# Optimization experiments

Hardware: AMD Instinct MI355X
Metric: run time of the kernel (lower is better)

Reference implementation:

```python
import jax, jax.numpy as jnp
import numpy as np

TOK = 256        # flattened batch*seq tokens (decode-style, memory-bound)
IN_F = 4096
OUT_F = 4096
N_OUTLIER = 32


def quantize_rowwise(x):
    """Symmetric rowwise int8 quantization: scale = rowwise absmax."""
    scale = jnp.max(jnp.abs(x), axis=-1)                      # [rows]
    safe = jnp.maximum(scale, 1e-8)
    q = jnp.clip(jnp.round(x / safe[:, None] * 127.0), -127.0, 127.0)
    return q, scale


def setup_inputs() -> dict:
    key = jax.random.key(0)
    k1, k2, k3, k4, k5 = jax.random.split(key, 5)
    x = jax.random.normal(k1, (TOK, IN_F), jnp.float32)
    weight_int8 = jax.random.randint(k2, (OUT_F, IN_F), -127, 128, jnp.int32)
    weight_scales = jax.random.uniform(k3, (OUT_F,), jnp.float32, minval=0.5, maxval=2.0)
    # spread unique outlier column indices across in_features
    outlier_indices = jnp.arange(N_OUTLIER, dtype=jnp.int32) * (IN_F // N_OUTLIER)
    outlier_weights = jax.random.normal(k4, (OUT_F, N_OUTLIER), jnp.float32) * 0.02
    bias = jax.random.normal(k5, (OUT_F,), jnp.float32) * 0.01
    # from_linear zeros outlier columns of the int8 weight before quantization
    weight_int8 = weight_int8.at[:, outlier_indices].set(0)
    return {"x": x, "weight_int8": weight_int8, "weight_scales": weight_scales,
            "outlier_indices": outlier_indices, "outlier_weights": outlier_weights,
            "bias": bias}


def reference(x, weight_int8, weight_scales, outlier_indices, outlier_weights, bias):
    # _forward_mixed: outlier columns handled in fp, rest quantize->dequant int8.
    # Selecting the non-outlier columns is equivalent to zeroing the outlier
    # columns (the dropped weight columns contribute 0 to the GEMM, and the
    # rowwise absmax scale is unaffected since |0| = 0). This keeps shapes
    # static and jit-friendly while computing identical math.
    in_f = x.shape[-1]
    mask = jnp.ones((in_f,), dtype=bool).at[outlier_indices].set(False)

    x_main = x * mask                                         # [T, in]
    xq, xs = quantize_rowwise(x_main)                         # int8-valued fp, [T]
    x_fp = xq * (xs[:, None] / 127.0)                         # dequantized activations

    w_fp = (weight_int8 * mask).astype(jnp.float32) * (weight_scales[:, None] / 127.0)  # [out, in]
    out_main = x_fp @ w_fp.T                                  # [T, out]

    x_outlier = x[:, outlier_indices]                         # [T, n_out]
    out_outlier = x_outlier @ outlier_weights.T               # [T, out]

    return out_main + out_outlier + bias
```

## Files before the change

### kernel.cpp

```cpp
#include <hip/hip_runtime.h>
#include <stdint.h>

#define TOK 256
#define IN_F 4096
#define OUT_F 4096
#define N_OUT 32

#define BN 16
#define MACRO_K 512
#define NMACRO (IN_F / MACRO_K)
#define KSTEPS (MACRO_K / 64)

typedef int v4i __attribute__((ext_vector_type(4)));

__global__ __launch_bounds__(256) void oal_quant(
    const float* __restrict__ x, const int* __restrict__ oidx,
    int8_t* __restrict__ xq, float* __restrict__ xs, float* __restrict__ xo)
{
    const int row = blockIdx.x;
    const int tid = threadIdx.x;
    __shared__ unsigned char flags[IN_F];
    __shared__ float wmax[4];
    __shared__ float s_scale;

    *reinterpret_cast<uint4*>(&flags[tid * 16]) = make_uint4(0u, 0u, 0u, 0u);
    __syncthreads();
    if (tid < N_OUT) flags[oidx[tid]] = 1;
    __syncthreads();

    const float* xr = x + (size_t)row * IN_F;
    float4 v[4];
    const float4* xp = reinterpret_cast<const float4*>(xr + tid * 16);
    #pragma unroll
    for (int i = 0; i < 4; ++i) v[i] = xp[i];

    uint4 f = *reinterpret_cast<const uint4*>(&flags[tid * 16]);
    unsigned int fw[4] = { f.x, f.y, f.z, f.w };
    float vals[16];
    #pragma unroll
    for (int i = 0; i < 4; ++i) {
        vals[i*4+0] = ((fw[i]      ) & 255u) ? 0.0f : v[i].x;
        vals[i*4+1] = ((fw[i] >>  8) & 255u) ? 0.0f : v[i].y;
        vals[i*4+2] = ((fw[i] >> 16) & 255u) ? 0.0f : v[i].z;
        vals[i*4+3] = ((fw[i] >> 24) & 255u) ? 0.0f : v[i].w;
    }

    float m = 0.0f;
    #pragma unroll
    for (int i = 0; i < 16; ++i) m = fmaxf(m, fabsf(vals[i]));
    #pragma unroll
    for (int off = 32; off > 0; off >>= 1) m = fmaxf(m, __shfl_xor(m, off, 64));
    const int lane = tid & 63, wid = tid >> 6;
    if (lane == 0) wmax[wid] = m;
    __syncthreads();
    if (tid == 0) {
        float s = fmaxf(fmaxf(wmax[0], wmax[1]), fmaxf(wmax[2], wmax[3]));
        s_scale = s;
        xs[row] = s;
    }
    __syncthreads();
    const float safe = fmaxf(s_scale, 1e-8f);

    int q[16];
    #pragma unroll
    for (int i = 0; i < 16; ++i) {
        float t = vals[i] / safe * 127.0f;
        t = fminf(127.0f, fmaxf(-127.0f, rintf(t)));
        q[i] = (int)t;
    }
    uint4 packed;
    unsigned int* pw = &packed.x;
    #pragma unroll
    for (int i = 0; i < 4; ++i)
        pw[i] = (unsigned)(q[i*4] & 255) | ((unsigned)(q[i*4+1] & 255) << 8)
              | ((unsigned)(q[i*4+2] & 255) << 16) | ((unsigned)(q[i*4+3] & 255) << 24);
    *reinterpret_cast<uint4*>(xq + (size_t)row * IN_F + tid * 16) = packed;

    if (tid < N_OUT) xo[row * N_OUT + tid] = xr[oidx[tid]];
}

__global__ __launch_bounds__(512, 2) void oal_gemm(
    const int8_t* __restrict__ xq, const int* __restrict__ w,
    const float* __restrict__ xs, const float* __restrict__ wscale,
    const float* __restrict__ ow, const float* __restrict__ bias,
    const float* __restrict__ xo, float* __restrict__ out)
{
    const int bn = blockIdx.x;
    const int tid = threadIdx.x;
    const int lane = tid & 63;
    const int wv = tid >> 6;

    __shared__ __align__(16) signed char Bs[2][BN][528];
    __shared__ __align__(16) float XO[TOK][N_OUT];

    {
        const float4* src = reinterpret_cast<const float4*>(xo);
        float4* dst = reinterpret_cast<float4*>(&XO[0][0]);
        #pragma unroll
        for (int i = 0; i < 4; ++i) dst[tid * 4 + i] = src[tid * 4 + i];
    }

    const int sr = tid >> 5;
    const int sc = tid & 31;
    const int* wbase = w + (size_t)(bn * BN + sr) * IN_F + sc * 16;

    int4 wr_[4];
    auto load_regs = [&](int mm) {
        const int4* p = reinterpret_cast<const int4*>(wbase + mm * MACRO_K);
        #pragma unroll
        for (int i = 0; i < 4; ++i) wr_[i] = p[i];
    };
    auto pack_store = [&](int buf) {
        int p[4];
        #pragma unroll
        for (int i = 0; i < 4; ++i) {
            int4 a = wr_[i];
            p[i] = (a.x & 255) | ((a.y & 255) << 8) | ((a.z & 255) << 16) | ((a.w & 255) << 24);
        }
        *reinterpret_cast<int4*>(&Bs[buf][sr][sc * 16]) = make_int4(p[0], p[1], p[2], p[3]);
    };

    const int mrow = wv * 32;
    const int koff_lane = (lane >> 4) * 16;
    const int8_t* a0p = xq + (size_t)(mrow + (lane & 15)) * IN_F + koff_lane;
    const int8_t* a1p = a0p + 16 * IN_F;

    v4i acc0 = {0, 0, 0, 0}, acc1 = {0, 0, 0, 0};

    load_regs(0);
    pack_store(0);
    load_regs(1);
    __syncthreads();

    #pragma unroll
    for (int mm = 0; mm < NMACRO; ++mm) {
        const int cur = mm & 1;
        #pragma unroll
        for (int kk = 0; kk < KSTEPS; ++kk) {
            const int kg = mm * MACRO_K + kk * 64;
            v4i av0 = *reinterpret_cast<const v4i*>(a0p + kg);
            v4i av1 = *reinterpret_cast<const v4i*>(a1p + kg);
            v4i bv  = *reinterpret_cast<const v4i*>(&Bs[cur][lane & 15][kk * 64 + koff_lane]);
            acc0 = __builtin_amdgcn_mfma_i32_16x16x64_i8(av0, bv, acc0, 0, 0, 0);
            acc1 = __builtin_amdgcn_mfma_i32_16x16x64_i8(av1, bv, acc1, 0, 0, 0);
        }
        if (mm < NMACRO - 1) {
            pack_store(cur ^ 1);
            if (mm < NMACRO - 2) load_regs(mm + 2);
            __syncthreads();
        }
    }

    const int ocol = bn * BN + (lane & 15);
    const float wsc = wscale[ocol] * (1.0f / 16129.0f);
    const float bo  = bias[ocol];
    float4 owr[8];
    const float4* owp = reinterpret_cast<const float4*>(ow + (size_t)ocol * N_OUT);
    #pragma unroll
    for (int i = 0; i < 8; ++i) owr[i] = owp[i];

    const int rbase = (lane >> 4) * 4;
    #pragma unroll
    for (int mt = 0; mt < 2; ++mt) {
        v4i a = mt ? acc1 : acc0;
        #pragma unroll
        for (int r = 0; r < 4; ++r) {
            const int t = mrow + mt * 16 + rbase + r;
            const float* xr2 = &XO[t][0];
            float dot = 0.0f;
            #pragma unroll
            for (int j = 0; j < 8; ++j) {
                float4 o4 = owr[j];
                dot += xr2[j*4+0]*o4.x + xr2[j*4+1]*o4.y + xr2[j*4+2]*o4.z + xr2[j*4+3]*o4.w;
            }
            out[(size_t)t * OUT_F + ocol] = (float)a[r] * (xs[t] * wsc) + bo + dot;
        }
    }
}

extern "C" void kernel_launch(void* const* d_in, const int* in_sizes, int n_in,
                              void* d_out, int out_size, void* d_ws, size_t ws_size,
                              hipStream_t stream) {
    const float* x      = (const float*)d_in[0];
    const int*   w      = (const int*)  d_in[1];
    const float* wscale = (const float*)d_in[2];
    const int*   oidx   = (const int*)  d_in[3];
    const float* ow     = (const float*)d_in[4];
    const float* bias   = (const float*)d_in[5];
    float* out = (float*)d_out;

    int8_t* xq = (int8_t*)d_ws;
    float*  xs = (float*)((char*)d_ws + (size_t)TOK * IN_F);
    float*  xo = (float*)((char*)d_ws + (size_t)TOK * IN_F + 1024);

    oal_quant<<<TOK, 256, 0, stream>>>(x, oidx, xq, xs, xo);
    oal_gemm<<<OUT_F / BN, 512, 0, stream>>>(xq, w, xs, wscale, ow, bias, xo, out);
}
```

Baseline: 138.8 us.

## Split-K int8 GEMM with 128-wide tiles, LDS direct loads, separate epilogue

Replaces the 16-column-per-block GEMM with 128x256 tiles split eight ways along K (256 blocks). Activations are quantized into a pre-tiled layout and streamed into LDS with global_load_lds, and weights are packed into a swizzled LDS layout. The kernel uses 32x32x32 int8 MFMAs with a 2x2 fragment per wave. Partial int32 sums go to workspace, or are atomically added into the output if workspace is too small, and a new epilogue kernel applies the scales, outlier dot product and bias. This improves weight and activation reuse and parallelism, at the cost of extra partial-sum traffic (8x the output size) and one more kernel launch.

```diff
diff --git a/kernel.cpp b/kernel.cpp
--- a/kernel.cpp
+++ b/kernel.cpp
@@ -6,16 +6,17 @@
 #define OUT_F 4096
 #define N_OUT 32
 
-#define BN 16
-#define MACRO_K 512
-#define NMACRO (IN_F / MACRO_K)
-#define KSTEPS (MACRO_K / 64)
-
-typedef int v4i __attribute__((ext_vector_type(4)));
+typedef int v4i  __attribute__((ext_vector_type(4)));
+typedef int v16i __attribute__((ext_vector_type(16)));
+
+__device__ __forceinline__ void gll16(const void* g, void* l) {
+    __builtin_amdgcn_global_load_lds((const __attribute__((address_space(1))) void*)g,
+                                     (__attribute__((address_space(3))) void*)l, 16, 0, 0);
+}
 
 __global__ __launch_bounds__(256) void oal_quant(
     const float* __restrict__ x, const int* __restrict__ oidx,
-    int8_t* __restrict__ xq, float* __restrict__ xs, float* __restrict__ xo)
+    int8_t* __restrict__ xqt, float* __restrict__ xs, float* __restrict__ xo)
 {
     const int row = blockIdx.x;
     const int tid = threadIdx.x;
@@ -23,16 +24,16 @@
     __shared__ float wmax[4];
     __shared__ float s_scale;
 
-    *reinterpret_cast<uint4*>(&flags[tid * 16]) = make_uint4(0u, 0u, 0u, 0u);
-    __syncthreads();
-    if (tid < N_OUT) flags[oidx[tid]] = 1;
-    __syncthreads();
-
     const float* xr = x + (size_t)row * IN_F;
     float4 v[4];
     const float4* xp = reinterpret_cast<const float4*>(xr + tid * 16);
     #pragma unroll
     for (int i = 0; i < 4; ++i) v[i] = xp[i];
+
+    *reinterpret_cast<uint4*>(&flags[tid * 16]) = make_uint4(0u, 0u, 0u, 0u);
+    __syncthreads();
+    if (tid < N_OUT) flags[oidx[tid]] = 1;
+    __syncthreads();
 
     uint4 f = *reinterpret_cast<const uint4*>(&flags[tid * 16]);
     unsigned int fw[4] = { f.x, f.y, f.z, f.w };
@@ -74,107 +75,170 @@
     for (int i = 0; i < 4; ++i)
         pw[i] = (unsigned)(q[i*4] & 255) | ((unsigned)(q[i*4+1] & 255) << 8)
               | ((unsigned)(q[i*4+2] & 255) << 16) | ((unsigned)(q[i*4+3] & 255) << 24);
-    *reinterpret_cast<uint4*>(xq + (size_t)row * IN_F + tid * 16) = packed;
+
+    const int ks32  = tid >> 1;
+    const int khalf = tid & 1;
+    const int rowgrp = row >> 5;
+    *reinterpret_cast<uint4*>(xqt + (size_t)ks32 * 8192 + rowgrp * 1024
+                              + (khalf * 32 + (row & 31)) * 16) = packed;
 
     if (tid < N_OUT) xo[row * N_OUT + tid] = xr[oidx[tid]];
 }
 
-__global__ __launch_bounds__(512, 2) void oal_gemm(
-    const int8_t* __restrict__ xq, const int* __restrict__ w,
+template<int MODE>
+__global__ __launch_bounds__(512, 1) void oal_gemm(
+    const int8_t* __restrict__ xqt, const int* __restrict__ wgt,
+    int* __restrict__ pout)
+{
+    __shared__ __align__(16) int8_t sm[131072];
+    int8_t* As = sm;
+    int8_t* Bs = sm + 65536;
+
+    const int bn = blockIdx.x;
+    const int ntile = bn & 31, kslice = bn >> 5;
+    const int n0 = ntile * 128;
+    const int tid = threadIdx.x, lane = tid & 63, wv = tid >> 6;
+    const int mg = wv & 3, ng = wv >> 2;
+    const int l31 = lane & 31, lh = lane >> 5;
+
+    auto issueA = [&](int h) {
+        const int8_t* s = xqt + ((size_t)(kslice * 16 + h * 4) << 13) + tid * 16;
+        int8_t* d = As + ((h & 1) << 15) + tid * 16;
+        gll16(s, d);
+        gll16(s + 8192, d + 8192);
+        gll16(s + 16384, d + 16384);
+        gll16(s + 24576, d + 24576);
+    };
+    issueA(0);
+
+    {
+        const int cbase = wv * 16;
+        #pragma unroll
+        for (int g = 0; g < 4; ++g) {
+            int4 t[8];
+            #pragma unroll
+            for (int j = 0; j < 8; ++j) {
+                const int q = g * 8 + j;
+                const int c = cbase + (q & 15);
+                const int ih = q >> 4;
+                t[j] = *reinterpret_cast<const int4*>(
+                    wgt + (size_t)(n0 + c) * IN_F + kslice * 512 + ih * 256 + lane * 4);
+            }
+            #pragma unroll
+            for (int j = 0; j < 8; ++j) {
+                const int q = g * 8 + j;
+                const int c = cbase + (q & 15);
+                const int ih = q >> 4;
+                unsigned pk = (unsigned)((t[j].x & 255) | ((t[j].y & 255) << 8)
+                             | ((t[j].z & 255) << 16) | ((t[j].w & 255) << 24));
+                const int ks32l = ih * 8 + (lane >> 3);
+                const int addr = ks32l * 4096 + (c >> 5) * 1024
+                               + (((lane >> 2) & 1) * 32 + ((c & 31) ^ (lane >> 3))) * 16
+                               + (lane & 3) * 4;
+                *reinterpret_cast<unsigned*>(Bs + addr) = pk;
+            }
+        }
+    }
+    __syncthreads();
+
+    v16i acc00 = {}, acc01 = {}, acc10 = {}, acc11 = {};
+    const int aoff = (2 * mg) * 1024 + lane * 16;
+    #pragma unroll
+    for (int h = 0; h < 4; ++h) {
+        if (h < 3) issueA(h + 1);
+        const int8_t* At = As + ((h & 1) << 15);
+        #pragma unroll
+        for (int loc = 0; loc < 4; ++loc) {
+            const int ks32g = h * 4 + loc;
+            const int s7 = ks32g & 7;
+            const int8_t* Ap = At + loc * 8192 + aoff;
+            const int8_t* Bp = Bs + ks32g * 4096 + (lh * 32 + (l31 ^ s7)) * 16;
+            v4i a0 = *reinterpret_cast<const v4i*>(Ap);
+            v4i a1 = *reinterpret_cast<const v4i*>(Ap + 1024);
+            v4i b0 = *reinterpret_cast<const v4i*>(Bp + (2 * ng) * 1024);
+            v4i b1 = *reinterpret_cast<const v4i*>(Bp + (2 * ng + 1) * 1024);
+            acc00 = __builtin_amdgcn_mfma_i32_32x32x32_i8(a0, b0, acc00, 0, 0, 0);
+            acc01 = __builtin_amdgcn_mfma_i32_32x32x32_i8(a0, b1, acc01, 0, 0, 0);
+            acc10 = __builtin_amdgcn_mfma_i32_32x32x32_i8(a1, b0, acc10, 0, 0, 0);
+            acc11 = __builtin_amdgcn_mfma_i32_32x32x32_i8(a1, b1, acc11, 0, 0, 0);
+        }
+        if (h < 3) __syncthreads();
+    }
+
+    const int colb = n0 + ng * 64 + l31;
+    const int rowb = mg * 64 + 4 * lh;
+#define OUTW(ACC, MF, NF) { _Pragma("unroll") \
+    for (int r = 0; r < 16; ++r) { \
+        const int rr = rowb + (MF)*32 + (r & 3) + ((r >> 2) << 3); \
+        const size_t off = (size_t)rr * OUT_F + colb + (NF)*32; \
+        if (MODE == 0) pout[(size_t)kslice * ((size_t)TOK * OUT_F) + off] = ACC[r]; \
+        else atomicAdd(pout + off, ACC[r]); \
+    } }
+    OUTW(acc00,0,0) OUTW(acc01,0,1) OUTW(acc10,1,0) OUTW(acc11,1,1)
+#undef OUTW
+}
+
+template<int MODE>
+__global__ __launch_bounds__(256) void oal_epi(
+    float* __restrict__ outp, const int* __restrict__ part,
     const float* __restrict__ xs, const float* __restrict__ wscale,
     const float* __restrict__ ow, const float* __restrict__ bias,
-    const float* __restrict__ xo, float* __restrict__ out)
+    const float* __restrict__ xo)
 {
-    const int bn = blockIdx.x;
+    const int rb = blockIdx.x >> 3;
+    const int cb = blockIdx.x & 7;
     const int tid = threadIdx.x;
-    const int lane = tid & 63;
-    const int wv = tid >> 6;
-
-    __shared__ __align__(16) signed char Bs[2][BN][528];
-    __shared__ __align__(16) float XO[TOK][N_OUT];
-
-    {
-        const float4* src = reinterpret_cast<const float4*>(xo);
-        float4* dst = reinterpret_cast<float4*>(&XO[0][0]);
+    const int c0 = cb * 512 + tid * 2;
+
+    __shared__ float sxo[8][32];
+    __shared__ float sxs[8];
+    if (tid < 64) {
+        const int rr = tid >> 3, jj = tid & 7;
+        *reinterpret_cast<float4*>(&sxo[rr][jj * 4]) =
+            *reinterpret_cast<const float4*>(xo + (size_t)(rb * 8 + rr) * N_OUT + jj * 4);
+    }
+    if (tid < 8) sxs[tid] = xs[rb * 8 + tid];
+    __syncthreads();
+
+    float o0[32], o1[32];
+    #pragma unroll
+    for (int j = 0; j < 8; ++j) {
+        float4 f0 = reinterpret_cast<const float4*>(ow + (size_t)c0 * N_OUT)[j];
+        float4 f1 = reinterpret_cast<const float4*>(ow + (size_t)(c0 + 1) * N_OUT)[j];
+        o0[j*4+0]=f0.x; o0[j*4+1]=f0.y; o0[j*4+2]=f0.z; o0[j*4+3]=f0.w;
+        o1[j*4+0]=f1.x; o1[j*4+1]=f1.y; o1[j*4+2]=f1.z; o1[j*4+3]=f1.w;
+    }
+    const float wsc0 = wscale[c0]     * (1.0f / 16129.0f);
+    const float wsc1 = wscale[c0 + 1] * (1.0f / 16129.0f);
+    const float bo0 = bias[c0], bo1 = bias[c0 + 1];
+
+    #pragma unroll
+    for (int r = 0; r < 8; ++r) {
+        const int row = rb * 8 + r;
+        const size_t off = (size_t)row * OUT_F + c0;
+        int px = 0, py = 0;
+        if (MODE == 0) {
+            #pragma unroll
+            for (int s2 = 0; s2 < 8; ++s2) {
+                int2 t = *reinterpret_cast<const int2*>(
+                    part + (size_t)s2 * ((size_t)TOK * OUT_F) + off);
+                px += t.x; py += t.y;
+            }
+        } else {
+            int2 t = *reinterpret_cast<const int2*>(reinterpret_cast<const int*>(outp) + off);
+            px = t.x; py = t.y;
+        }
+        float d0 = 0.f, d1 = 0.f;
         #pragma unroll
-        for (int i = 0; i < 4; ++i) dst[tid * 4 + i] = src[tid * 4 + i];
-    }
-
-    const int sr = tid >> 5;
-    const int sc = tid & 31;
-    const int* wbase = w + (size_t)(bn * BN + sr) * IN_F + sc * 16;
-
-    int4 wr_[4];
-    auto load_regs = [&](int mm) {
-        const int4* p = reinterpret_cast<const int4*>(wbase + mm * MACRO_K);
-        #pragma unroll
-        for (int i = 0; i < 4; ++i) wr_[i] = p[i];
-    };
-    auto pack_store = [&](int buf) {
-        int p[4];
-        #pragma unroll
-        for (int i = 0; i < 4; ++i) {
-            int4 a = wr_[i];
-            p[i] = (a.x & 255) | ((a.y & 255) << 8) | ((a.z & 255) << 16) | ((a.w & 255) << 24);
-        }
-        *reinterpret_cast<int4*>(&Bs[buf][sr][sc * 16]) = make_int4(p[0], p[1], p[2], p[3]);
-    };
-
-    const int mrow = wv * 32;
-    const int koff_lane = (lane >> 4) * 16;
-    const int8_t* a0p = xq + (size_t)(mrow + (lane & 15)) * IN_F + koff_lane;
-    const int8_t* a1p = a0p + 16 * IN_F;
-
-    v4i acc0 = {0, 0, 0, 0}, acc1 = {0, 0, 0, 0};
-
-    load_regs(0);
-    pack_store(0);
-    load_regs(1);
-    __syncthreads();
-
-    #pragma unroll
-    for (int mm = 0; mm < NMACRO; ++mm) {
-        const int cur = mm & 1;
-        #pragma unroll
-        for (int kk = 0; kk < KSTEPS; ++kk) {
-            const int kg = mm * MACRO_K + kk * 64;
-            v4i av0 = *reinterpret_cast<const v4i*>(a0p + kg);
-            v4i av1 = *reinterpret_cast<const v4i*>(a1p + kg);
-            v4i bv  = *reinterpret_cast<const v4i*>(&Bs[cur][lane & 15][kk * 64 + koff_lane]);
-            acc0 = __builtin_amdgcn_mfma_i32_16x16x64_i8(av0, bv, acc0, 0, 0, 0);
-            acc1 = __builtin_amdgcn_mfma_i32_16x16x64_i8(av1, bv, acc1, 0, 0, 0);
-        }
-        if (mm < NMACRO - 1) {
-            pack_store(cur ^ 1);
-            if (mm < NMACRO - 2) load_regs(mm + 2);
-            __syncthreads();
-        }
-    }
-
-    const int ocol = bn * BN + (lane & 15);
-    const float wsc = wscale[ocol] * (1.0f / 16129.0f);
-    const float bo  = bias[ocol];
-    float4 owr[8];
-    const float4* owp = reinterpret_cast<const float4*>(ow + (size_t)ocol * N_OUT);
-    #pragma unroll
-    for (int i = 0; i < 8; ++i) owr[i] = owp[i];
-
-    const int rbase = (lane >> 4) * 4;
-    #pragma unroll
-    for (int mt = 0; mt < 2; ++mt) {
-        v4i a = mt ? acc1 : acc0;
-        #pragma unroll
-        for (int r = 0; r < 4; ++r) {
-            const int t = mrow + mt * 16 + rbase + r;
-            const float* xr2 = &XO[t][0];
-            float dot = 0.0f;
-            #pragma unroll
-            for (int j = 0; j < 8; ++j) {
-                float4 o4 = owr[j];
-                dot += xr2[j*4+0]*o4.x + xr2[j*4+1]*o4.y + xr2[j*4+2]*o4.z + xr2[j*4+3]*o4.w;
-            }
-            out[(size_t)t * OUT_F + ocol] = (float)a[r] * (xs[t] * wsc) + bo + dot;
-        }
+        for (int k = 0; k < 32; ++k) {
+            const float xv = sxo[r][k];
+            d0 += xv * o0[k]; d1 += xv * o1[k];
+        }
+        const float s = sxs[r];
+        float2 res;
+        res.x = (float)px * (s * wsc0) + d0 + bo0;
+        res.y = (float)py * (s * wsc1) + d1 + bo1;
+        *reinterpret_cast<float2*>(outp + off) = res;
     }
 }
 
@@ -189,10 +253,19 @@
     const float* bias   = (const float*)d_in[5];
     float* out = (float*)d_out;
 
-    int8_t* xq = (int8_t*)d_ws;
-    float*  xs = (float*)((char*)d_ws + (size_t)TOK * IN_F);
-    float*  xo = (float*)((char*)d_ws + (size_t)TOK * IN_F + 1024);
-
-    oal_quant<<<TOK, 256, 0, stream>>>(x, oidx, xq, xs, xo);
-    oal_gemm<<<OUT_F / BN, 512, 0, stream>>>(xq, w, xs, wscale, ow, bias, xo, out);
-}
+    int8_t* xqt = (int8_t*)d_ws;
+    float*  xs  = (float*)((char*)d_ws + (1 << 20));
+    float*  xo  = (float*)((char*)d_ws + (1 << 20) + 1024);
+    int*    P2  = (int*)  ((char*)d_ws + (1 << 20) + 1024 + 32768);
+    const size_t need = (size_t)(1 << 20) + 1024 + 32768 + (size_t)8 * TOK * OUT_F * 4;
+
+    oal_quant<<<TOK, 256, 0, stream>>>(x, oidx, xqt, xs, xo);
+    if (ws_size >= need) {
+        oal_gemm<0><<<256, 512, 0, stream>>>(xqt, w, P2);
+        oal_epi<0><<<256, 256, 0, stream>>>(out, P2, xs, wscale, ow, bias, xo);
+    } else {
+        hipMemsetAsync(d_out, 0, (size_t)TOK * OUT_F * 4, stream);
+        oal_gemm<1><<<256, 512, 0, stream>>>(xqt, w, (int*)d_out);
+        oal_epi<1><<<256, 256, 0, stream>>>(out, (const int*)d_out, xs, wscale, ow, bias, xo);
+    }
+}
```

New measurement: 122.8 us. 11.5% less time.
